# Kernel optimization log

Hardware: AMD Instinct MI355X
Metric: run time of the kernel (lower is better)

Reference implementation:

```python
import jax, jax.numpy as jnp
import numpy as np

B, S, H = 8, 4096, 2048
HINT, WS, STRIDE = 4, 16, 8
MLP_H = 64


def _window_starts():
    # Mirrors the torch loop: break when the window is shorter than window_size//2.
    starts = []
    for s in range(0, S, STRIDE):
        e = min(s + WS, S)
        if e - s < WS // 2:
            break
        starts.append(s)
    return np.asarray(starts, dtype=np.int32)  # [W] = [512]


def setup_inputs() -> dict:
    key = jax.random.key(0)
    k1, k2, k3, k4, k5 = jax.random.split(key, 5)
    return {
        "hidden_states": jax.random.normal(k1, (B, S, H), jnp.float32),
        "attention_mask": jax.random.randint(k2, (B, S), 0, 2).astype(jnp.int32),
        "hint_features": jax.random.normal(k3, (B, S, HINT), jnp.float32),
        "W1": jax.random.normal(k4, (H + HINT, MLP_H), jnp.float32) * 0.02,
        "b1": jnp.zeros((MLP_H,), jnp.float32),
        "W2": jax.random.normal(k5, (MLP_H, 1), jnp.float32) * 0.02,
        "b2": jnp.zeros((1,), jnp.float32),
    }


def reference(hidden_states, attention_mask, hint_features, W1, b1, W2, b2):
    starts = jnp.asarray(_window_starts())               # [W]
    idx = starts[:, None] + jnp.arange(WS)               # [W, ws]
    pos_valid = (idx < S).astype(jnp.float32)            # [W, ws]  (pads past seq end)
    idxc = jnp.minimum(idx, S - 1)

    # [B, W, ws] combined attention + in-bounds mask
    mask = attention_mask[:, idxc].astype(jnp.float32) * pos_valid[None]
    denom = jnp.clip(jnp.sum(mask, axis=-1, keepdims=True), 1.0, None)  # [B, W, 1]

    # Gather overlapping windows once, pool with a single einsum each.
    win_h = hidden_states[:, idxc]                        # [B, W, ws, H]
    win_f = hint_features[:, idxc]                        # [B, W, ws, HINT]
    pooled_h = jnp.einsum('bwk,bwkh->bwh', mask, win_h) / denom
    pooled_f = jnp.einsum('bwk,bwkh->bwh', mask, win_f) / denom
    pooled = jnp.concatenate([pooled_h, pooled_f], axis=-1)  # [B, W, H+HINT]

    # MLP (dropout is identity at inference); torch GELU default = exact erf.
    h = jax.nn.gelu(pooled @ W1 + b1, approximate=False)
    window_logits = (h @ W2 + b2)[..., 0]                 # [B, W]
    window_mask = (jnp.sum(mask, axis=-1) > 0).astype(jnp.float32)  # [B, W]
    return window_logits, window_mask
```

## Files before the change

kernel.cpp:

```cpp
#include <hip/hip_runtime.h>
#include <math.h>

#define B_      8
#define S_      4096
#define H_      2048
#define HINT_   4
#define WS_     16
#define STRIDE_ 8
#define MLPH_   64
#define NW_     512
#define WPB_    8
#define ROWS_   72
#define KT_     68
#define KPAD_   2176
#define LDK_    2184
#define NT_     4
#define PLD_    66

typedef float  floatx4 __attribute__((ext_vector_type(4)));
typedef short  shortx8 __attribute__((ext_vector_type(8)));

__device__ __forceinline__ unsigned short f2b(float x) {
    unsigned u = __float_as_uint(x);
    u += 0x7FFFu + ((u >> 16) & 1u);
    return (unsigned short)(u >> 16);
}

__global__ void prep_w1(const float* __restrict__ W1, unsigned short* __restrict__ W1B) {
    const int blk  = blockIdx.x;
    const int nt   = blk / KT_;
    const int kt   = blk % KT_;
    const int lane = threadIdx.x;
    const int n     = nt * 16 + (lane & 15);
    const int kbase = kt * 32 + (lane >> 4) * 8;
    unsigned short tmp[8];
#pragma unroll
    for (int j = 0; j < 8; ++j) {
        const int k = kbase + j;
        const float v = (k < (H_ + HINT_)) ? W1[(size_t)k * MLPH_ + n] : 0.0f;
        tmp[j] = f2b(v);
    }
    *(uint4*)(W1B + (((size_t)nt * KT_ + kt) * 64 + lane) * 8) = *(const uint4*)tmp;
}

__global__ __launch_bounds__(512, 6) void wbh_kernel(
    const float* __restrict__ hidden,
    const int*   __restrict__ amask,
    const float* __restrict__ hintf,
    const float* __restrict__ b1,
    const float* __restrict__ W2,
    const float* __restrict__ b2,
    const unsigned short* __restrict__ W1B,
    float* __restrict__ out)
{
    __shared__ unsigned short pooledLds[WPB_ * LDK_];
    __shared__ float amLds[ROWS_];
    __shared__ float rinvLds[WPB_];
    __shared__ float partLds[WPB_ * PLD_];

    const int tid = threadIdx.x;
    const int bid = blockIdx.x;
    const int gid   = (bid & 7) * 64 + (bid >> 3);
    const int b     = gid >> 6;
    const int chunk = gid & 63;
    const int w0    = chunk * WPB_;
    const int s0    = chunk * (WPB_ * STRIDE_);

    if (tid < 8 * 62) {
        const int row = tid / 62, cc = tid % 62;
        *(unsigned*)&pooledLds[row * LDK_ + 2052 + cc * 2] = 0u;
    }
    if (tid < ROWS_) {
        const int p = s0 + tid;
        amLds[tid] = (p < S_) ? (float)amask[b * S_ + p] : 0.0f;
    }
    __syncthreads();

    if (tid < WPB_) {
        float s = 0.f;
#pragma unroll
        for (int k = 0; k < WS_; ++k) s += amLds[tid * STRIDE_ + k];
        rinvLds[tid] = 1.0f / fmaxf(s, 1.0f);
        out[(size_t)(B_ * NW_) + (size_t)b * NW_ + w0 + tid] = (s > 0.f) ? 1.0f : 0.0f;
    }
    __syncthreads();

    const int c0 = tid * 4;
    const float* rowBase = hidden + ((size_t)b * S_ + s0) * H_ + c0;

    floatx4 prev = (floatx4){0.f, 0.f, 0.f, 0.f};
#pragma unroll
    for (int g = 0; g <= WPB_; ++g) {
        float am[STRIDE_];
        const float* ptr[STRIDE_];
#pragma unroll
        for (int k = 0; k < STRIDE_; ++k) {
            const int rr = g * STRIDE_ + k;
            am[k]  = amLds[rr];
            ptr[k] = (am[k] != 0.0f) ? (rowBase + (size_t)rr * H_) : rowBase;
        }
        floatx4 v[STRIDE_];
#pragma unroll
        for (int k = 0; k < STRIDE_; ++k) v[k] = *(const floatx4*)ptr[k];

        floatx4 cur = (floatx4){0.f, 0.f, 0.f, 0.f};
#pragma unroll
        for (int k = 0; k < STRIDE_; ++k) {
            cur.x = fmaf(am[k], v[k].x, cur.x);
            cur.y = fmaf(am[k], v[k].y, cur.y);
            cur.z = fmaf(am[k], v[k].z, cur.z);
            cur.w = fmaf(am[k], v[k].w, cur.w);
        }
        if (g >= 1) {
            const int w = g - 1;
            const floatx4 s = prev + cur;
            const float r = rinvLds[w];
            unsigned short q[4];
            q[0] = f2b(s.x * r); q[1] = f2b(s.y * r);
            q[2] = f2b(s.z * r); q[3] = f2b(s.w * r);
            *(uint2*)(&pooledLds[w * LDK_ + c0]) = *(const uint2*)q;
        }
        prev = cur;
    }

    if (tid < WPB_ * HINT_) {
        const int w = tid >> 2, hc = tid & 3;
        float s = 0.f;
#pragma unroll
        for (int k = 0; k < WS_; ++k) {
            const int rr = w * STRIDE_ + k;
            const float amv = amLds[rr];
            float hv = 0.f;
            if (amv != 0.0f)
                hv = hintf[((size_t)b * S_ + (s0 + rr)) * HINT_ + hc];
            s += amv * hv;
        }
        pooledLds[w * LDK_ + H_ + hc] = f2b(s * rinvLds[w]);
    }
    __syncthreads();

    const int wid  = tid >> 6;
    const int lane = tid & 63;
    if (wid < NT_) {
        floatx4 dacc = (floatx4){0.f, 0.f, 0.f, 0.f};
        const unsigned short* aBase = pooledLds + (lane & 7) * LDK_ + (lane >> 4) * 8;
        const unsigned short* bBase = W1B + ((size_t)wid * KT_ * 64 + lane) * 8;
#pragma unroll 4
        for (int kt = 0; kt < KT_; ++kt) {
            const shortx8 af = *(const shortx8*)(aBase + kt * 32);
            const shortx8 bf = *(const shortx8*)(bBase + (size_t)kt * 64 * 8);
            dacc = __builtin_amdgcn_mfma_f32_16x16x32_bf16(af, bf, dacc, 0, 0, 0);
        }
        if (lane < 32) {
            const int m0 = (lane >> 4) * 4;
            const int j  = wid * 16 + (lane & 15);
#pragma unroll
            for (int r = 0; r < 4; ++r)
                partLds[(m0 + r) * PLD_ + j] = dacc[r];
        }
    }
    __syncthreads();

    {
        const int m = tid >> 6;
        const int j = tid & 63;
        const float a = partLds[m * PLD_ + j] + b1[j];
        float g = 0.5f * a * (1.0f + erff(a * 0.70710678118654752f)) * W2[j];
#pragma unroll
        for (int off = 32; off > 0; off >>= 1) g += __shfl_down(g, off, 64);
        if (j == 0) out[(size_t)b * NW_ + w0 + m] = g + b2[0];
    }
}

extern "C" void kernel_launch(void* const* d_in, const int* in_sizes, int n_in,
                              void* d_out, int out_size, void* d_ws, size_t ws_size,
                              hipStream_t stream) {
    const float* hidden = (const float*)d_in[0];
    const int*   amask  = (const int*)d_in[1];
    const float* hintf  = (const float*)d_in[2];
    const float* W1     = (const float*)d_in[3];
    const float* b1     = (const float*)d_in[4];
    const float* W2     = (const float*)d_in[5];
    const float* b2     = (const float*)d_in[6];
    float* out          = (float*)d_out;

    unsigned short* W1B = (unsigned short*)d_ws;

    prep_w1<<<NT_ * KT_, 64, 0, stream>>>(W1, W1B);
    wbh_kernel<<<B_ * (NW_ / WPB_), 512, 0, stream>>>(
        hidden, amask, hintf, b1, W2, b2, W1B, out);
}
```

Baseline: 348.3 us.

## Split pooling and MLP into separate kernels via global bf16 pooled buffer

```diff
diff --git a/kernel.cpp b/kernel.cpp
--- a/kernel.cpp
+++ b/kernel.cpp
@@ -13,12 +13,13 @@
 #define ROWS_   72
 #define KT_     68
 #define KPAD_   2176
-#define LDK_    2184
 #define NT_     4
-#define PLD_    66
+#define PLD2_   65
 
 typedef float  floatx4 __attribute__((ext_vector_type(4)));
 typedef short  shortx8 __attribute__((ext_vector_type(8)));
+
+#define W1B_BYTE_OFF 18874368
 
 __device__ __forceinline__ unsigned short f2b(float x) {
     unsigned u = __float_as_uint(x);
@@ -43,20 +44,15 @@
     *(uint4*)(W1B + (((size_t)nt * KT_ + kt) * 64 + lane) * 8) = *(const uint4*)tmp;
 }
 
-__global__ __launch_bounds__(512, 6) void wbh_kernel(
+__global__ __launch_bounds__(512, 6) void pool_kernel(
     const float* __restrict__ hidden,
     const int*   __restrict__ amask,
     const float* __restrict__ hintf,
-    const float* __restrict__ b1,
-    const float* __restrict__ W2,
-    const float* __restrict__ b2,
-    const unsigned short* __restrict__ W1B,
+    unsigned short* __restrict__ pooled,
     float* __restrict__ out)
 {
-    __shared__ unsigned short pooledLds[WPB_ * LDK_];
     __shared__ float amLds[ROWS_];
     __shared__ float rinvLds[WPB_];
-    __shared__ float partLds[WPB_ * PLD_];
 
     const int tid = threadIdx.x;
     const int bid = blockIdx.x;
@@ -65,15 +61,16 @@
     const int chunk = gid & 63;
     const int w0    = chunk * WPB_;
     const int s0    = chunk * (WPB_ * STRIDE_);
-
-    if (tid < 8 * 62) {
-        const int row = tid / 62, cc = tid % 62;
-        *(unsigned*)&pooledLds[row * LDK_ + 2052 + cc * 2] = 0u;
-    }
+    const int gw0   = b * NW_ + w0;
+
     if (tid < ROWS_) {
         const int p = s0 + tid;
         amLds[tid] = (p < S_) ? (float)amask[b * S_ + p] : 0.0f;
     }
+    if (tid < 8 * 62) {
+        const int row = tid / 62, cc = tid % 62;
+        *(unsigned*)&pooled[(size_t)(gw0 + row) * KPAD_ + 2052 + cc * 2] = 0u;
+    }
     __syncthreads();
 
     if (tid < WPB_) {
@@ -86,22 +83,23 @@
     __syncthreads();
 
     const int c0 = tid * 4;
-    const float* rowBase = hidden + ((size_t)b * S_ + s0) * H_ + c0;
+    const float* __restrict__ base = hidden + (size_t)b * S_ * H_;
+    const unsigned rowOff0 = (unsigned)(s0 * H_ + c0);
 
     floatx4 prev = (floatx4){0.f, 0.f, 0.f, 0.f};
 #pragma unroll
     for (int g = 0; g <= WPB_; ++g) {
-        float am[STRIDE_];
-        const float* ptr[STRIDE_];
+        float    am [STRIDE_];
+        unsigned off[STRIDE_];
 #pragma unroll
         for (int k = 0; k < STRIDE_; ++k) {
             const int rr = g * STRIDE_ + k;
             am[k]  = amLds[rr];
-            ptr[k] = (am[k] != 0.0f) ? (rowBase + (size_t)rr * H_) : rowBase;
+            off[k] = (am[k] != 0.0f) ? rowOff0 + (unsigned)(rr * H_) : rowOff0;
         }
         floatx4 v[STRIDE_];
 #pragma unroll
-        for (int k = 0; k < STRIDE_; ++k) v[k] = *(const floatx4*)ptr[k];
+        for (int k = 0; k < STRIDE_; ++k) v[k] = *(const floatx4*)(base + off[k]);
 
         floatx4 cur = (floatx4){0.f, 0.f, 0.f, 0.f};
 #pragma unroll
@@ -118,7 +116,7 @@
             unsigned short q[4];
             q[0] = f2b(s.x * r); q[1] = f2b(s.y * r);
             q[2] = f2b(s.z * r); q[3] = f2b(s.w * r);
-            *(uint2*)(&pooledLds[w * LDK_ + c0]) = *(const uint2*)q;
+            *(uint2*)(&pooled[(size_t)(gw0 + w) * KPAD_ + c0]) = *(const uint2*)q;
         }
         prev = cur;
     }
@@ -135,40 +133,58 @@
                 hv = hintf[((size_t)b * S_ + (s0 + rr)) * HINT_ + hc];
             s += amv * hv;
         }
-        pooledLds[w * LDK_ + H_ + hc] = f2b(s * rinvLds[w]);
-    }
-    __syncthreads();
-
+        pooled[(size_t)(gw0 + w) * KPAD_ + H_ + hc] = f2b(s * rinvLds[w]);
+    }
+}
+
+__global__ __launch_bounds__(512, 2) void mlp_kernel(
+    const unsigned short* __restrict__ pooled,
+    const unsigned short* __restrict__ W1B,
+    const float* __restrict__ b1,
+    const float* __restrict__ W2,
+    const float* __restrict__ b2,
+    float* __restrict__ out)
+{
+    __shared__ float partLds[32 * PLD2_];
+
+    const int tid  = threadIdx.x;
     const int wid  = tid >> 6;
     const int lane = tid & 63;
-    if (wid < NT_) {
-        floatx4 dacc = (floatx4){0.f, 0.f, 0.f, 0.f};
-        const unsigned short* aBase = pooledLds + (lane & 7) * LDK_ + (lane >> 4) * 8;
-        const unsigned short* bBase = W1B + ((size_t)wid * KT_ * 64 + lane) * 8;
+    const int blk  = blockIdx.x;
+    const int mrow = (wid & 1) * 16;
+    const int nt   = wid >> 1;
+
+    const unsigned short* aBase =
+        pooled + (size_t)(blk * 32 + mrow + (lane & 15)) * KPAD_ + (lane >> 4) * 8;
+    const unsigned short* bBase = W1B + ((size_t)nt * KT_ * 64 + lane) * 8;
+
+    floatx4 dacc = (floatx4){0.f, 0.f, 0.f, 0.f};
 #pragma unroll 4
-        for (int kt = 0; kt < KT_; ++kt) {
-            const shortx8 af = *(const shortx8*)(aBase + kt * 32);
-            const shortx8 bf = *(const shortx8*)(bBase + (size_t)kt * 64 * 8);
-            dacc = __builtin_amdgcn_mfma_f32_16x16x32_bf16(af, bf, dacc, 0, 0, 0);
-        }
-        if (lane < 32) {
-            const int m0 = (lane >> 4) * 4;
-            const int j  = wid * 16 + (lane & 15);
-#pragma unroll
-            for (int r = 0; r < 4; ++r)
-                partLds[(m0 + r) * PLD_ + j] = dacc[r];
-        }
+    for (int kt = 0; kt < KT_; ++kt) {
+        const shortx8 af = *(const shortx8*)(aBase + kt * 32);
+        const shortx8 bf = *(const shortx8*)(bBase + (size_t)kt * 512);
+        dacc = __builtin_amdgcn_mfma_f32_16x16x32_bf16(af, bf, dacc, 0, 0, 0);
+    }
+    {
+        const int r0 = mrow + (lane >> 4) * 4;
+        const int c  = nt * 16 + (lane & 15);
+        partLds[(r0 + 0) * PLD2_ + c] = dacc[0];
+        partLds[(r0 + 1) * PLD2_ + c] = dacc[1];
+        partLds[(r0 + 2) * PLD2_ + c] = dacc[2];
+        partLds[(r0 + 3) * PLD2_ + c] = dacc[3];
     }
     __syncthreads();
 
-    {
-        const int m = tid >> 6;
-        const int j = tid & 63;
-        const float a = partLds[m * PLD_ + j] + b1[j];
-        float g = 0.5f * a * (1.0f + erff(a * 0.70710678118654752f)) * W2[j];
+    const float b1v = b1[lane];
+    const float w2v = W2[lane];
+#pragma unroll
+    for (int rr = 0; rr < 4; ++rr) {
+        const int row = wid * 4 + rr;
+        const float a = partLds[row * PLD2_ + lane] + b1v;
+        float g = 0.5f * a * (1.0f + erff(a * 0.70710678118654752f)) * w2v;
 #pragma unroll
         for (int off = 32; off > 0; off >>= 1) g += __shfl_down(g, off, 64);
-        if (j == 0) out[(size_t)b * NW_ + w0 + m] = g + b2[0];
+        if (lane == 0) out[(size_t)blk * 32 + row] = g + b2[0];
     }
 }
 
@@ -184,9 +200,10 @@
     const float* b2     = (const float*)d_in[6];
     float* out          = (float*)d_out;
 
-    unsigned short* W1B = (unsigned short*)d_ws;
+    unsigned short* pooled = (unsigned short*)d_ws;
+    unsigned short* W1B    = (unsigned short*)((char*)d_ws + W1B_BYTE_OFF);
 
     prep_w1<<<NT_ * KT_, 64, 0, stream>>>(W1, W1B);
-    wbh_kernel<<<B_ * (NW_ / WPB_), 512, 0, stream>>>(
-        hidden, amask, hintf, b1, W2, b2, W1B, out);
-}
+    pool_kernel<<<B_ * (NW_ / WPB_), 512, 0, stream>>>(hidden, amask, hintf, pooled, out);
+    mlp_kernel<<<(B_ * NW_) / 32, 512, 0, stream>>>(pooled, W1B, b1, W2, b2, out);
+}
```

Result: slower. 370.1 us (+6.3%).
